# Optimization experiments

Hardware: AMD Instinct MI355X
Metric: run time of the kernel (lower is better)

Reference implementation:

```python
import jax, jax.numpy as jnp
import numpy as np

D_MODEL = 2048
D_STATE = 64
D_CONV = 4
EXPAND = 2
HEADDIM = 64
NGROUPS = 1
CHUNK = 64
D_INNER = D_MODEL * EXPAND          # 4096
NHEADS = D_INNER // HEADDIM         # 64
D_IN_PROJ = 2 * D_INNER + 2 * NGROUPS * D_STATE + NHEADS
BATCH, SEQLEN = 2, 4096
RMS_EPS = 1e-6


def elu_plus_one(x):
    return jax.nn.elu(x) + 1.0


def softplus(x):
    return jnp.where(x > 20, x, jnp.log1p(jnp.exp(x)))


def causal_conv1d(x, w, b):
    # x: (B, L, D), w: (K, D) depthwise kernel, b: (D,)
    Bsz, L, Dn = x.shape
    k = w.shape[0]
    xp = jnp.transpose(jnp.pad(x, ((0, 0), (k - 1, 0), (0, 0))), (0, 2, 1))  # (B, D, L+K-1)
    kern = jnp.transpose(w, (1, 0))[:, None, :]  # (D, 1, K)
    y = jax.lax.conv_general_dilated(xp, kern, (1,), 'VALID',
                                     feature_group_count=Dn,
                                     dimension_numbers=('NCH', 'OIH', 'NCH'))
    return jnp.transpose(y, (0, 2, 1)) + b


def ssd_chunked(q, k, v, a, chunk_size):
    # SSD / chunked linear attention with per-step scalar decay.
    # Recurrence: h_t = a_t * h_{t-1} + k_t v_t^T ; y_t = q_t @ h_t
    # q,k: (B,H,L,N); v: (B,H,L,P); a: (B,H,L) in (0,1)
    Bsz, H, L, N = q.shape
    S = chunk_size
    C = L // S
    qc = q.reshape(Bsz, H, C, S, N)
    kc = k.reshape(Bsz, H, C, S, N)
    vc = v.reshape(Bsz, H, C, S, -1)
    la = jnp.log(a).reshape(Bsz, H, C, S)
    cs = jnp.cumsum(la, axis=-1)                 # inclusive cumsum of log-decay within chunk
    causal = jnp.tril(jnp.ones((S, S), bool))
    # decay from position j to i (j<=i): exp(cs_i - cs_j)
    logdec = jnp.where(causal, cs[..., :, None] - cs[..., None, :], -jnp.inf)
    att = jnp.einsum('bhcsn,bhctn->bhcst', qc, kc) * jnp.exp(logdec)
    y_intra = jnp.einsum('bhcst,bhctp->bhcsp', att, vc)
    total = cs[..., -1]                           # (B,H,C) total log-decay per chunk
    k_scaled = kc * jnp.exp(total[..., None, None] - cs[..., None])
    states = jnp.einsum('bhcsn,bhcsp->bhcnp', k_scaled, vc)  # per-chunk state update
    d_t = jnp.moveaxis(jnp.exp(total), 2, 0)      # (C,B,H)
    s_t = jnp.moveaxis(states, 2, 0)              # (C,B,H,N,P)

    def step(h, inp):
        d, s = inp
        return d[..., None, None] * h + s, h      # emit state at chunk start

    _, h_prev = jax.lax.scan(step, jnp.zeros_like(s_t[0]), (d_t, s_t))
    h_prev = jnp.moveaxis(h_prev, 0, 2)           # (B,H,C,N,P)
    y_inter = jnp.einsum('bhcsn,bhcnp->bhcsp', qc * jnp.exp(cs)[..., None], h_prev)
    return (y_intra + y_inter).reshape(Bsz, H, L, -1)


def setup_inputs() -> dict:
    key = jax.random.key(0)
    k0, k1, k2, k3 = jax.random.split(key, 4)
    u = jax.random.normal(k0, (BATCH, SEQLEN, D_MODEL), jnp.float32)
    in_proj_w = jax.random.normal(k1, (D_MODEL, D_IN_PROJ), jnp.float32) / np.sqrt(D_MODEL)
    conv_weight = jax.random.normal(k2, (D_CONV, D_INNER), jnp.float32) / np.sqrt(D_CONV)
    conv_bias = jnp.zeros((D_INNER,), jnp.float32)
    A_log = jnp.log(jnp.linspace(1.0, 16.0, NHEADS)).astype(jnp.float32)
    dt_init = jnp.exp(jnp.linspace(np.log(0.001), np.log(0.1), NHEADS))
    dt_bias = (dt_init + jnp.log(-jnp.expm1(-dt_init))).astype(jnp.float32)
    D_param = jnp.ones((NHEADS,), jnp.float32)
    norm_scale = jnp.ones((D_INNER,), jnp.float32)
    out_proj_w = jax.random.normal(k3, (D_INNER, D_MODEL), jnp.float32) / np.sqrt(D_INNER)
    return dict(u=u, in_proj_w=in_proj_w, conv_weight=conv_weight, conv_bias=conv_bias,
                A_log=A_log, dt_bias=dt_bias, D_param=D_param, norm_scale=norm_scale,
                out_proj_w=out_proj_w)


def reference(u, in_proj_w, conv_weight, conv_bias, A_log, dt_bias, D_param, norm_scale, out_proj_w):
    Bsz, L, _ = u.shape
    zxBCdt = u @ in_proj_w
    splits = [D_INNER, 2 * D_INNER, 2 * D_INNER + NGROUPS * D_STATE, 2 * D_INNER + 2 * NGROUPS * D_STATE]
    z, x, B_proj, C_proj, dt_logits = jnp.split(zxBCdt, splits, axis=-1)
    x = jax.nn.silu(causal_conv1d(x, conv_weight, conv_bias))
    B_mat = elu_plus_one(B_proj.reshape(Bsz, L, NGROUPS, D_STATE))
    C_mat = elu_plus_one(C_proj.reshape(Bsz, L, NGROUPS, D_STATE))
    hpg = NHEADS // NGROUPS
    B_mat = jnp.repeat(B_mat, hpg, axis=2)   # (B,L,H,N)
    C_mat = jnp.repeat(C_mat, hpg, axis=2)
    dt = softplus(dt_logits + dt_bias)        # (B,L,H)
    a = jnp.exp(-dt * jnp.exp(A_log))         # (B,L,H), per-step decay
    x_heads = x.reshape(Bsz, L, NHEADS, HEADDIM)
    q = jnp.transpose(C_mat, (0, 2, 1, 3))
    k = jnp.transpose(B_mat, (0, 2, 1, 3))
    v = jnp.transpose(x_heads, (0, 2, 1, 3))
    a_t = jnp.transpose(a, (0, 2, 1))
    y = ssd_chunked(q, k, v, a_t, CHUNK)
    y = y + D_param[None, :, None, None] * v  # skip connection
    y = jnp.transpose(y, (0, 2, 1, 3)).reshape(Bsz, L, D_INNER)
    y = y * jax.lax.rsqrt(jnp.mean(y * y, axis=-1, keepdims=True) + RMS_EPS) * norm_scale
    y = y * jax.nn.silu(z)
    return y @ out_proj_w
```

## Files before the change

### kernel.cpp

```cpp
#include <hip/hip_runtime.h>
#include <hip/hip_bf16.h>
#include <cstdint>
#include <cstddef>

#define BATCH   2
#define SEQLEN  4096
#define DMODEL  2048
#define DINNER  4096
#define NHEADS  64
#define HEADDIM 64
#define DSTATE  64
#define CHUNK   64
#define NCHUNK  (SEQLEN/CHUNK)
#define DPROJ   8384
#define DPROJ_PAD 8448
#define MTOK    (BATCH*SEQLEN)
#define RMS_EPS 1e-6f

typedef __hip_bfloat16 bf16;
typedef __attribute__((ext_vector_type(8))) short bf16x8;
typedef __attribute__((ext_vector_type(4))) float f32x4;

__device__ __forceinline__ float siluf(float x) { return x / (1.f + expf(-x)); }
__device__ __forceinline__ float to_f(float x) { return x; }
__device__ __forceinline__ float to_f(bf16 x) { return __bfloat162float(x); }
__device__ __forceinline__ float bf2f(short s) { bf16 h; *(short*)&h = s; return __bfloat162float(h); }
__device__ __forceinline__ void from_f(float& d, float x) { d = x; }
__device__ __forceinline__ void from_f(bf16& d, float x) { d = __float2bfloat16(x); }

__device__ __forceinline__ void gload16(const void* g, void* l) {
  __builtin_amdgcn_global_load_lds(
      (const __attribute__((address_space(1))) void*)g,
      (__attribute__((address_space(3))) void*)l, 16, 0, 0);
}

template <typename TC, bool MASK, int KT>
__global__ __launch_bounds__(512, 2) void gemm_u(
    const bf16* __restrict__ A, int lda,
    const bf16* __restrict__ BT, int ldb,
    TC* __restrict__ C, int ldc, int Nvalid, int gx) {
  __shared__ __align__(16) bf16 As[4 * 8192];
  __shared__ __align__(16) bf16 Bs[4 * 8192];
  const int tid  = threadIdx.x;
  const int lane = tid & 63;
  const int w    = tid >> 6;
  const int wm   = w >> 2;
  const int wn   = w & 3;
  const int lr   = lane & 15, lg = lane >> 4;
  const int fo   = 8 * (lg ^ ((lr >> 1) & 3));

  int nwg = gridDim.x;
  int bid = (int)blockIdx.x;
  int idx = (bid & 7) * (nwg >> 3) + (bid >> 3);
  int spos = idx % (8 * gx);
  const int m0 = ((idx / (8 * gx)) * 8 + (spos & 7)) * 256;
  const int n0 = (spos >> 3) * 256;

  const int srow = tid >> 2;
  const int ce   = 8 * ((tid & 3) ^ ((tid >> 3) & 3));
  const bf16* pA0 = A  + (size_t)(m0 + srow)       * lda + ce;
  const bf16* pA1 = A  + (size_t)(m0 + 128 + srow) * lda + ce;
  const bf16* pB0 = BT + (size_t)(n0 + srow)       * ldb + ce;
  const bf16* pB1 = BT + (size_t)(n0 + 128 + srow) * ldb + ce;
  const int wofs = w * 512;
  const int aRd = (wm * 128 + lr) * 32 + fo;
  const int bRd = (wn * 64 + lr) * 32 + fo;

#define STAGE_A(kt) do {                                       \
    bf16* d_ = As + (((kt) & 3) << 13);  int kk_ = (kt) << 5;  \
    gload16(pA0 + kk_, d_ + wofs);                             \
    gload16(pA1 + kk_, d_ + 4096 + wofs);                      \
  } while (0)
#define STAGE_B(kt) do {                                       \
    bf16* d_ = Bs + (((kt) & 3) << 13);  int kk_ = (kt) << 5;  \
    gload16(pB0 + kk_, d_ + wofs);                             \
    gload16(pB1 + kk_, d_ + 4096 + wofs);                      \
  } while (0)

  f32x4 acc[8][4];
#pragma unroll
  for (int m = 0; m < 8; ++m)
#pragma unroll
    for (int n = 0; n < 4; ++n) acc[m][n] = (f32x4){0.f, 0.f, 0.f, 0.f};

#define KBODY(T, DOSTAGE, VMC) do {                                          \
    const bf16* Ab = As + (((T) & 3) << 13);                                 \
    const bf16* Bb = Bs + (((T) & 3) << 13);                                 \
    if (DOSTAGE) { STAGE_A((T) + 3); STAGE_B((T) + 3); }                     \
    bf16x8 bfv[4], af[4], ag[4];                                             \
    _Pragma("unroll")                                                        \
    for (int n = 0; n < 4; ++n) bfv[n] = *(const bf16x8*)&Bb[bRd + n * 512]; \
    _Pragma("unroll")                                                        \
    for (int m = 0; m < 4; ++m) af[m] = *(const bf16x8*)&Ab[aRd + m * 512];  \
    __builtin_amdgcn_sched_barrier(0);                                       \
    _Pragma("unroll")                                                        \
    for (int m = 0; m < 4; ++m) ag[m] = *(const bf16x8*)&Ab[aRd + (m + 4) * 512]; \
    asm volatile("s_waitcnt lgkmcnt(4)" ::: "memory");                       \
    __builtin_amdgcn_sched_barrier(0);                                       \
    __builtin_amdgcn_s_setprio(1);                                           \
    _Pragma("unroll")                                                        \
    for (int m = 0; m < 4; ++m)                                              \
      _Pragma("unroll")                                                      \
      for (int n = 0; n < 4; ++n)                                            \
        acc[m][n] = __builtin_amdgcn_mfma_f32_16x16x32_bf16(af[m], bfv[n], acc[m][n], 0, 0, 0); \
    asm volatile("s_waitcnt lgkmcnt(0)" ::: "memory");                       \
    __builtin_amdgcn_sched_barrier(0);                                       \
    _Pragma("unroll")                                                        \
    for (int m = 0; m < 4; ++m)                                              \
      _Pragma("unroll")                                                      \
      for (int n = 0; n < 4; ++n)                                            \
        acc[m + 4][n] = __builtin_amdgcn_mfma_f32_16x16x32_bf16(ag[m], bfv[n], acc[m + 4][n], 0, 0, 0); \
    __builtin_amdgcn_s_setprio(0);                                           \
    asm volatile("s_waitcnt vmcnt(" #VMC ")" ::: "memory");                  \
    __builtin_amdgcn_s_barrier();                                            \
    __builtin_amdgcn_sched_barrier(0);                                       \
  } while (0)

  STAGE_A(0); STAGE_B(0); STAGE_A(1); STAGE_B(1); STAGE_A(2); STAGE_B(2);
  asm volatile("s_waitcnt vmcnt(8)" ::: "memory");
  __builtin_amdgcn_s_barrier();
  __builtin_amdgcn_sched_barrier(0);

#pragma unroll 4
  for (int t = 0; t < KT - 3; ++t) KBODY(t, true, 8);
  KBODY(KT - 3, false, 4);
  KBODY(KT - 2, false, 0);
  KBODY(KT - 1, false, 0);
#undef KBODY
#undef STAGE_A
#undef STAGE_B

  if constexpr (__is_same(TC, bf16)) {
    bf16* Ws = (w < 4 ? As : Bs) + (w & 3) * 8192;
#pragma unroll
    for (int m = 0; m < 8; ++m)
#pragma unroll
      for (int n = 0; n < 4; ++n)
#pragma unroll
        for (int reg = 0; reg < 4; ++reg) {
          int row = m * 16 + lg * 4 + reg;
          int slot = (n * 2 + (lr >> 3)) ^ (row & 7);
          Ws[row * 64 + slot * 8 + (lr & 7)] = __float2bfloat16(acc[m][n][reg]);
        }
    asm volatile("s_waitcnt lgkmcnt(0)" ::: "memory");
#pragma unroll
    for (int i = 0; i < 16; ++i) {
      int row = i * 8 + (lane >> 3);
      bf16x8 v = *(const bf16x8*)&Ws[row * 64 + ((lane & 7) ^ (lane >> 3)) * 8];
      int gcol = n0 + wn * 64 + (lane & 7) * 8;
      if (!MASK || gcol < Nvalid)
        *(bf16x8*)&((bf16*)C)[(size_t)(m0 + wm * 128 + row) * ldc + gcol] = v;
    }
  } else {
#pragma unroll
    for (int m = 0; m < 8; ++m)
#pragma unroll
      for (int n = 0; n < 4; ++n) {
        int col = n0 + wn * 64 + n * 16 + lr;
        if (MASK && col >= Nvalid) continue;
        size_t rbase = (size_t)(m0 + wm * 128 + m * 16 + lg * 4);
#pragma unroll
        for (int reg = 0; reg < 4; ++reg)
          from_f(C[(rbase + reg) * ldc + col], acc[m][n][reg]);
      }
  }
}

template <typename TC, bool MASK>
__global__ __launch_bounds__(256) void gemm_mfma(
    const bf16* __restrict__ A, int lda,
    const bf16* __restrict__ BT, int ldb,
    TC* __restrict__ C, int ldc, int Kdim, int Nvalid) {
  __shared__ __align__(16) bf16 As[128 * 32];
  __shared__ __align__(16) bf16 Bs[128 * 32];
  const int tid  = threadIdx.x;
  const int lane = tid & 63;
  const int w    = tid >> 6;
  const int m0 = blockIdx.y * 128;
  const int n0 = blockIdx.x * 128;

  const int rs0 = w * 32 + (lane >> 2);
  const int ce  = 8 * ((lane & 3) ^ ((lane >> 2) & 3));
  const int fo  = 8 * ((lane >> 4) ^ (lane & 3));
  const int lr  = lane & 15, lg = lane >> 4;
  const int wr = w >> 1, wc = w & 1;

  f32x4 acc[4][4];
#pragma unroll
  for (int m = 0; m < 4; ++m)
#pragma unroll
    for (int n = 0; n < 4; ++n) acc[m][n] = (f32x4){0.f, 0.f, 0.f, 0.f};

  const size_t arow0 = (size_t)(m0 + rs0) * lda;
  const size_t arow1 = (size_t)(m0 + rs0 + 16) * lda;
  const size_t brow0 = (size_t)(n0 + rs0) * ldb;
  const size_t brow1 = (size_t)(n0 + rs0 + 16) * ldb;
  bf16* lA0 = &As[(w * 2 + 0) * 512];
  bf16* lA1 = &As[(w * 2 + 1) * 512];
  bf16* lB0 = &Bs[(w * 2 + 0) * 512];
  bf16* lB1 = &Bs[(w * 2 + 1) * 512];

  for (int k0 = 0; k0 < Kdim; k0 += 32) {
    __syncthreads();
    gload16(A + arow0 + k0 + ce, lA0);
    gload16(A + arow1 + k0 + ce, lA1);
    gload16(BT + brow0 + k0 + ce, lB0);
    gload16(BT + brow1 + k0 + ce, lB1);
    __syncthreads();
    bf16x8 af[4], bfr[4];
#pragma unroll
    for (int m = 0; m < 4; ++m)
      af[m] = *(const bf16x8*)&As[(wr * 64 + m * 16 + lr) * 32 + fo];
#pragma unroll
    for (int n = 0; n < 4; ++n)
      bfr[n] = *(const bf16x8*)&Bs[(wc * 64 + n * 16 + lr) * 32 + fo];
#pragma unroll
    for (int m = 0; m < 4; ++m)
#pragma unroll
      for (int n = 0; n < 4; ++n)
        acc[m][n] = __builtin_amdgcn_mfma_f32_16x16x32_bf16(af[m], bfr[n], acc[m][n], 0, 0, 0);
  }

#pragma unroll
  for (int m = 0; m < 4; ++m)
#pragma unroll
    for (int n = 0; n < 4; ++n) {
      int col = n0 + wc * 64 + n * 16 + lr;
      if (MASK && col >= Nvalid) continue;
      size_t rbase = (size_t)(m0 + wr * 64 + m * 16 + lg * 4);
#pragma unroll
      for (int reg = 0; reg < 4; ++reg)
        from_f(C[(rbase + reg) * ldc + col], acc[m][n][reg]);
    }
}

__global__ __launch_bounds__(256) void cast_bf16_kernel(
    const float* __restrict__ x, bf16* __restrict__ y) {
  size_t i = ((size_t)blockIdx.x * 256 + threadIdx.x) * 4;
  float4 v = *(const float4*)(x + i);
  y[i + 0] = __float2bfloat16(v.x);
  y[i + 1] = __float2bfloat16(v.y);
  y[i + 2] = __float2bfloat16(v.z);
  y[i + 3] = __float2bfloat16(v.w);
}

__global__ __launch_bounds__(256) void transpose_cast_kernel(
    const float* __restrict__ W, bf16* __restrict__ WT, int N, int K) {
  __shared__ float t[32][33];
  int n0 = blockIdx.x * 32, k0 = blockIdx.y * 32;
  int tx = threadIdx.x & 31, ty = threadIdx.x >> 5;
#pragma unroll
  for (int i = 0; i < 4; ++i) {
    int n = n0 + tx;
    t[ty + i * 8][tx] = (n < N) ? W[(size_t)(k0 + ty + i * 8) * N + n] : 0.f;
  }
  __syncthreads();
#pragma unroll
  for (int i = 0; i < 4; ++i) {
    int nn = ty + i * 8;
    WT[(size_t)(n0 + nn) * K + k0 + tx] = __float2bfloat16(t[tx][nn]);
  }
}

__global__ __launch_bounds__(256) void conv_silu_kernel(
    const bf16* __restrict__ zx, const float* __restrict__ cw,
    const float* __restrict__ cb, bf16* __restrict__ xc) {
  int idx = blockIdx.x * 256 + threadIdx.x;
  int d8 = (idx & 511) * 8;
  int m = idx >> 9;
  int l = m & (SEQLEN - 1);
  int b = m >> 12;
  float acc[8];
#pragma unroll
  for (int j = 0; j < 8; ++j) acc[j] = cb[d8 + j];
#pragma unroll
  for (int k = 0; k < 4; ++k) {
    int li = l - 3 + k;
    if (li >= 0) {
      bf16x8 xv = *(const bf16x8*)&zx[(size_t)(b * SEQLEN + li) * DPROJ + DINNER + d8];
      const float* cwp = cw + k * DINNER + d8;
#pragma unroll
      for (int j = 0; j < 8; ++j) acc[j] += bf2f(xv[j]) * cwp[j];
    }
  }
  bf16x8 o;
#pragma unroll
  for (int j = 0; j < 8; ++j) { bf16 h = __float2bfloat16(siluf(acc[j])); o[j] = *(short*)&h; }
  *(bf16x8*)&xc[(size_t)m * DINNER + d8] = o;
}

__global__ __launch_bounds__(256) void prep_kernel(
    const bf16* __restrict__ zx, const float* __restrict__ A_log,
    const float* __restrict__ dt_bias, bf16* __restrict__ Bmb,
    bf16* __restrict__ Cmb, float* __restrict__ la) {
  int idx = blockIdx.x * 256 + threadIdx.x;
  int j = idx & 63;
  int m = idx >> 6;
  const bf16* row = zx + (size_t)m * DPROJ;
  float bv = to_f(row[2 * DINNER + j]);
  float cv = to_f(row[2 * DINNER + DSTATE + j]);
  float dtl = to_f(row[2 * DINNER + 2 * DSTATE + j]) + dt_bias[j];
  from_f(Bmb[idx], bv > 0.f ? bv + 1.f : expf(bv));
  from_f(Cmb[idx], cv > 0.f ? cv + 1.f : expf(cv));
  float dt = dtl > 20.f ? dtl : log1pf(expf(dtl));
  la[idx] = -dt * expf(A_log[j]);
}

__global__ __launch_bounds__(64) void cumsum_kernel(
    const float* __restrict__ la, float* __restrict__ cs) {
  int bid = blockIdx.x;
  int c = bid & 63, h = (bid >> 6) & 63, b = bid >> 12;
  int s = threadIdx.x;
  __shared__ float lds[64];
  size_t base = (size_t)(b * SEQLEN + c * CHUNK + s) * 64 + h;
  lds[s] = la[base];
  __syncthreads();
  float acc = 0.f;
  for (int t = 0; t <= s; ++t) acc += lds[t];
  cs[base] = acc;
}

__global__ __launch_bounds__(256) void states_mfma(
    const bf16* __restrict__ Bmb, const bf16* __restrict__ xc,
    const float* __restrict__ cs, bf16* __restrict__ st) {
  int bid = blockIdx.x;
  int c = bid & 63, h = (bid >> 6) & 63, b = bid >> 12;
  int m0 = b * SEQLEN + c * CHUNK;
  int tid = threadIdx.x, lane = tid & 63, w = tid >> 6;
  int lr = lane & 15, lg = lane >> 4;
  __shared__ bf16 vT[64 * 72];
  __shared__ bf16 kT[64 * 72];
  int s4 = tid >> 2, c16 = (tid & 3) * 16;
  float cstot = cs[(size_t)(m0 + 63) * 64 + h];
  float ws = expf(cstot - cs[(size_t)(m0 + s4) * 64 + h]);
  {
    union { bf16x8 v[2]; bf16 hh[16]; } u;
    const bf16x8* pv = (const bf16x8*)&xc[(size_t)(m0 + s4) * DINNER + h * 64 + c16];
    u.v[0] = pv[0]; u.v[1] = pv[1];
#pragma unroll
    for (int i = 0; i < 16; ++i) vT[(c16 + i) * 72 + s4] = u.hh[i];
    const bf16x8* pk = (const bf16x8*)&Bmb[(size_t)(m0 + s4) * 64 + c16];
    u.v[0] = pk[0]; u.v[1] = pk[1];
#pragma unroll
    for (int i = 0; i < 16; ++i) kT[(c16 + i) * 72 + s4] = __float2bfloat16(to_f(u.hh[i]) * ws);
  }
  __syncthreads();
  f32x4 acc[4];
#pragma unroll
  for (int ct = 0; ct < 4; ++ct) acc[ct] = (f32x4){0.f, 0.f, 0.f, 0.f};
#pragma unroll
  for (int ks = 0; ks < 2; ++ks) {
    bf16x8 af = *(const bf16x8*)&vT[(w * 16 + lr) * 72 + ks * 32 + lg * 8];
#pragma unroll
    for (int ct = 0; ct < 4; ++ct) {
      bf16x8 bf_ = *(const bf16x8*)&kT[(ct * 16 + lr) * 72 + ks * 32 + lg * 8];
      acc[ct] = __builtin_amdgcn_mfma_f32_16x16x32_bf16(af, bf_, acc[ct], 0, 0, 0);
    }
  }
  size_t ob = (((size_t)(b * NHEADS + h)) * NCHUNK + c) * 4096;
#pragma unroll
  for (int ct = 0; ct < 4; ++ct) {
    int n = ct * 16 + lr;
#pragma unroll
    for (int r = 0; r < 4; ++r) {
      int p = w * 16 + lg * 4 + r;
      from_f(st[ob + (size_t)p * 64 + n], acc[ct][r]);
    }
  }
}

__global__ __launch_bounds__(256) void scan_kernel(
    const float* __restrict__ cs, bf16* __restrict__ st) {
  int bid = blockIdx.x;
  int bh = bid >> 2, qq = bid & 3;
  int b = bh >> 6, h = bh & 63;
  int tid = threadIdx.x;
  __shared__ float dec[64];
  if (tid < 64)
    dec[tid] = expf(cs[(size_t)(b * SEQLEN + tid * CHUNK + 63) * 64 + h]);
  int e0 = qq * 1024 + tid * 4;
  float hr[4] = {0.f, 0.f, 0.f, 0.f};
  size_t base = (size_t)bh * NCHUNK * 4096;
  typedef __attribute__((ext_vector_type(4))) short bf16x4;
  union U { bf16x4 v; bf16 hh[4]; };
  U buf[4];
  buf[0].v = *(bf16x4*)(st + base + 0 * 4096 + e0);
  buf[1].v = *(bf16x4*)(st + base + 1 * 4096 + e0);
  buf[2].v = *(bf16x4*)(st + base + 2 * 4096 + e0);
  __syncthreads();
#pragma unroll 4
  for (int c = 0; c < NCHUNK; ++c) {
    if (c + 3 < NCHUNK)
      buf[(c + 3) & 3].v = *(bf16x4*)(st + base + (size_t)(c + 3) * 4096 + e0);
    float d = dec[c];
    U out;
#pragma unroll
    for (int i = 0; i < 4; ++i) {
      float sv = to_f(buf[c & 3].hh[i]);
      from_f(out.hh[i], hr[i]);
      hr[i] = d * hr[i] + sv;
    }
    *(bf16x4*)(st + base + (size_t)c * 4096 + e0) = out.v;
  }
}

__global__ __launch_bounds__(256) void chunk_out_mfma(
    const bf16* __restrict__ Bmb, const bf16* __restrict__ Cmb,
    const bf16* __restrict__ xc, const float* __restrict__ cs,
    const bf16* __restrict__ st, const float* __restrict__ Dp,
    bf16* __restrict__ zx) {
  int bid = blockIdx.x;
  int c = bid & 63, h = (bid >> 6) & 63, b = bid >> 12;
  int m0 = b * SEQLEN + c * CHUNK;
  int tid = threadIdx.x, lane = tid & 63, w = tid >> 6;
  int lr = lane & 15, lg = lane >> 4;
  __shared__ bf16 qL[64 * 72];
  __shared__ bf16 kL[64 * 72];
  __shared__ bf16 A2[64 * 136];
  __shared__ bf16 B2[64 * 136];
  __shared__ float csl[64];
  int s4 = tid >> 2, c16 = (tid & 3) * 16;

  if (tid < 64) csl[tid] = cs[(size_t)(m0 + tid) * 64 + h];
  {
    const bf16x8* pq = (const bf16x8*)&Cmb[(size_t)(m0 + s4) * 64 + c16];
    *(bf16x8*)&qL[s4 * 72 + c16] = pq[0];
    *(bf16x8*)&qL[s4 * 72 + c16 + 8] = pq[1];
    const bf16x8* pk = (const bf16x8*)&Bmb[(size_t)(m0 + s4) * 64 + c16];
    *(bf16x8*)&kL[s4 * 72 + c16] = pk[0];
    *(bf16x8*)&kL[s4 * 72 + c16 + 8] = pk[1];
  }
  {
    union { bf16x8 v[2]; bf16 hh[16]; } u;
    const bf16x8* pv = (const bf16x8*)&xc[(size_t)(m0 + s4) * DINNER + h * 64 + c16];
    u.v[0] = pv[0]; u.v[1] = pv[1];
#pragma unroll
    for (int i = 0; i < 16; ++i) B2[(c16 + i) * 136 + s4] = u.hh[i];
  }
  {
    size_t hb = (((size_t)(b * NHEADS + h)) * NCHUNK + c) * 4096;
    const bf16x8* ph = (const bf16x8*)&st[hb + (size_t)s4 * 64 + c16];
    *(bf16x8*)&B2[s4 * 136 + 64 + c16] = ph[0];
    *(bf16x8*)&B2[s4 * 136 + 64 + c16 + 8] = ph[1];
  }
  __syncthreads();

  f32x4 acc1[4];
#pragma unroll
  for (int ct = 0; ct < 4; ++ct) acc1[ct] = (f32x4){0.f, 0.f, 0.f, 0.f};
#pragma unroll
  for (int ks = 0; ks < 2; ++ks) {
    bf16x8 af = *(const bf16x8*)&qL[(w * 16 + lr) * 72 + ks * 32 + lg * 8];
#pragma unroll
    for (int ct = 0; ct < 4; ++ct) {
      bf16x8 bf_ = *(const bf16x8*)&kL[(ct * 16 + lr) * 72 + ks * 32 + lg * 8];
      acc1[ct] = __builtin_amdgcn_mfma_f32_16x16x32_bf16(af, bf_, acc1[ct], 0, 0, 0);
    }
  }
  {
    float es = expf(csl[s4]);
    union { bf16x8 v[2]; bf16 hh[16]; } u;
    const bf16x8* pq = (const bf16x8*)&qL[s4 * 72 + c16];
    u.v[0] = pq[0]; u.v[1] = pq[1];
#pragma unroll
    for (int i = 0; i < 16; ++i) u.hh[i] = __float2bfloat16(to_f(u.hh[i]) * es);
    *(bf16x8*)&A2[s4 * 136 + 64 + c16] = u.v[0];
    *(bf16x8*)&A2[s4 * 136 + 64 + c16 + 8] = u.v[1];
  }
#pragma unroll
  for (int ct = 0; ct < 4; ++ct) {
    int t = ct * 16 + lr;
#pragma unroll
    for (int r = 0; r < 4; ++r) {
      int s = w * 16 + lg * 4 + r;
      float val = (t <= s) ? acc1[ct][r] * expf(csl[s] - csl[t]) : 0.f;
      A2[s * 136 + t] = __float2bfloat16(val);
    }
  }
  __syncthreads();

  float Dh = Dp[h];
  f32x4 acc2[4];
#pragma unroll
  for (int ct = 0; ct < 4; ++ct) {
    int p = ct * 16 + lr;
#pragma unroll
    for (int r = 0; r < 4; ++r)
      acc2[ct][r] = Dh * to_f(B2[p * 136 + (w * 16 + lg * 4 + r)]);
  }
#pragma unroll
  for (int ks = 0; ks < 4; ++ks) {
    bf16x8 af = *(const bf16x8*)&A2[(w * 16 + lr) * 136 + ks * 32 + lg * 8];
#pragma unroll
    for (int ct = 0; ct < 4; ++ct) {
      bf16x8 bf_ = *(const bf16x8*)&B2[(ct * 16 + lr) * 136 + ks * 32 + lg * 8];
      acc2[ct] = __builtin_amdgcn_mfma_f32_16x16x32_bf16(af, bf_, acc2[ct], 0, 0, 0);
    }
  }
  __syncthreads();
#pragma unroll
  for (int ct = 0; ct < 4; ++ct) {
    int p = ct * 16 + lr;
#pragma unroll
    for (int r = 0; r < 4; ++r)
      qL[(w * 16 + lg * 4 + r) * 72 + p] = __float2bfloat16(acc2[ct][r]);
  }
  __syncthreads();
  {
    const bf16x8* py = (const bf16x8*)&qL[s4 * 72 + c16];
    bf16x8* pg = (bf16x8*)&zx[(size_t)(m0 + s4) * DPROJ + DINNER + h * 64 + c16];
    pg[0] = py[0]; pg[1] = py[1];
  }
}

__global__ __launch_bounds__(256) void rmsnorm_gate_kernel(
    bf16* __restrict__ zx, const float* __restrict__ scale) {
  int m = blockIdx.x;
  int tid = threadIdx.x;
  bf16* row = zx + (size_t)m * DPROJ;
  float vals[16];
  float ss = 0.f;
#pragma unroll
  for (int g = 0; g < 2; ++g) {
    int d8 = (tid + g * 256) * 8;
    bf16x8 yv = *(const bf16x8*)&row[DINNER + d8];
#pragma unroll
    for (int j = 0; j < 8; ++j) {
      float y = bf2f(yv[j]);
      vals[g * 8 + j] = y;
      ss += y * y;
    }
  }
#pragma unroll
  for (int off = 32; off > 0; off >>= 1) ss += __shfl_down(ss, off, 64);
  __shared__ float red[4];
  if ((tid & 63) == 0) red[tid >> 6] = ss;
  __syncthreads();
  float tot = red[0] + red[1] + red[2] + red[3];
  float inv = rsqrtf(tot / (float)DINNER + RMS_EPS);
#pragma unroll
  for (int g = 0; g < 2; ++g) {
    int d8 = (tid + g * 256) * 8;
    bf16x8 zv = *(const bf16x8*)&row[d8];
    const float* sc = scale + d8;
    bf16x8 o;
#pragma unroll
    for (int j = 0; j < 8; ++j) {
      bf16 hh = __float2bfloat16(vals[g * 8 + j] * inv * sc[j] * siluf(bf2f(zv[j])));
      o[j] = *(short*)&hh;
    }
    *(bf16x8*)&row[DINNER + d8] = o;
  }
}

extern "C" void kernel_launch(void* const* d_in, const int* in_sizes, int n_in,
                              void* d_out, int out_size, void* d_ws, size_t ws_size,
                              hipStream_t stream) {
  const float* u       = (const float*)d_in[0];
  const float* Win     = (const float*)d_in[1];
  const float* cw      = (const float*)d_in[2];
  const float* cb      = (const float*)d_in[3];
  const float* A_log   = (const float*)d_in[4];
  const float* dt_bias = (const float*)d_in[5];
  const float* Dp      = (const float*)d_in[6];
  const float* nscale  = (const float*)d_in[7];
  const float* Wout    = (const float*)d_in[8];
  float* out = (float*)d_out;

  bf16* zx = (bf16*)d_ws;
  bf16* xc = zx + (size_t)MTOK * DPROJ;
  bf16* ub = xc;
  bf16* wT = xc + (size_t)MTOK * DINNER;
  bf16* Bmb = wT + (size_t)DPROJ_PAD * DMODEL;
  bf16* Cmb = Bmb + (size_t)MTOK * 64;
  float* la = (float*)(Cmb + (size_t)MTOK * 64);
  float* cs = la + (size_t)MTOK * 64;
  bf16* st = (bf16*)d_out;

  cast_bf16_kernel<<<(MTOK * DMODEL) / (256 * 4), 256, 0, stream>>>(u, ub);
  transpose_cast_kernel<<<dim3(DPROJ_PAD / 32, DMODEL / 32), 256, 0, stream>>>(Win, wT, DPROJ, DMODEL);
  gemm_u<bf16, false, DMODEL / 32><<<(2 * DINNER / 256) * (MTOK / 256), 512, 0, stream>>>(
      ub, DMODEL, wT, DMODEL, zx, DPROJ, DPROJ, 2 * DINNER / 256);
  gemm_mfma<bf16, true><<<dim3(2, MTOK / 128), 256, 0, stream>>>(
      ub, DMODEL, wT + (size_t)(2 * DINNER) * DMODEL, DMODEL,
      zx + 2 * DINNER, DPROJ, DMODEL, 2 * DINNER + 192 - (2 * DINNER));
  transpose_cast_kernel<<<dim3(DMODEL / 32, DINNER / 32), 256, 0, stream>>>(Wout, wT, DMODEL, DINNER);
  conv_silu_kernel<<<(MTOK * 512) / 256, 256, 0, stream>>>(zx, cw, cb, xc);
  prep_kernel<<<(MTOK * 64) / 256, 256, 0, stream>>>(zx, A_log, dt_bias, Bmb, Cmb, la);
  cumsum_kernel<<<BATCH * NHEADS * NCHUNK, 64, 0, stream>>>(la, cs);
  states_mfma<<<BATCH * NHEADS * NCHUNK, 256, 0, stream>>>(Bmb, xc, cs, st);
  scan_kernel<<<BATCH * NHEADS * 4, 256, 0, stream>>>(cs, st);
  chunk_out_mfma<<<BATCH * NHEADS * NCHUNK, 256, 0, stream>>>(Bmb, Cmb, xc, cs, st, Dp, zx);
  rmsnorm_gate_kernel<<<MTOK, 256, 0, stream>>>(zx, nscale);
  gemm_u<float, false, DINNER / 32><<<(DMODEL / 256) * (MTOK / 256), 512, 0, stream>>>(
      zx + DINNER, DPROJ, wT, DINNER, out, DMODEL, DMODEL, DMODEL / 256);
}
```

Measured before the change: 662.6 us.

## Add 16-wave GEMM for input projection and fuse prep with chunk cumsum

New measurement: 663.9 us. About the same (+0.2%).

```diff
diff --git a/kernel.cpp b/kernel.cpp
--- a/kernel.cpp
+++ b/kernel.cpp
@@ -32,6 +32,103 @@
   __builtin_amdgcn_global_load_lds(
       (const __attribute__((address_space(1))) void*)g,
       (__attribute__((address_space(3))) void*)l, 16, 0, 0);
+}
+
+template <int KT>
+__global__ __launch_bounds__(1024, 4) void gemm_w16(
+    const bf16* __restrict__ A, int lda,
+    const bf16* __restrict__ BT, int ldb,
+    bf16* __restrict__ C, int ldc, int gx) {
+  __shared__ __align__(16) bf16 As[4 * 8192];
+  __shared__ __align__(16) bf16 Bs[4 * 8192];
+  const int tid  = threadIdx.x;
+  const int lane = tid & 63;
+  const int w    = tid >> 6;
+  const int wm   = w >> 2;
+  const int wn   = w & 3;
+  const int lr   = lane & 15, lg = lane >> 4;
+  const int fo   = 8 * (lg ^ ((lr >> 1) & 3));
+
+  int nwg = gridDim.x;
+  int bid = (int)blockIdx.x;
+  int idx = (bid & 7) * (nwg >> 3) + (bid >> 3);
+  int spos = idx % (8 * gx);
+  const int m0 = ((idx / (8 * gx)) * 8 + (spos & 7)) * 256;
+  const int n0 = (spos >> 3) * 256;
+
+  const int srow = tid >> 2;
+  const int ce   = 8 * ((tid & 3) ^ ((tid >> 3) & 3));
+  const bf16* pA = A  + (size_t)(m0 + srow) * lda + ce;
+  const bf16* pB = BT + (size_t)(n0 + srow) * ldb + ce;
+  const int wofs = w * 512;
+  const int aRd = (wm * 64 + lr) * 32 + fo;
+  const int bRd = (wn * 64 + lr) * 32 + fo;
+
+#define STAGE_A(kt) gload16(pA + ((kt) << 5), As + (((kt) & 3) << 13) + wofs)
+#define STAGE_B(kt) gload16(pB + ((kt) << 5), Bs + (((kt) & 3) << 13) + wofs)
+
+  f32x4 acc[4][4];
+#pragma unroll
+  for (int m = 0; m < 4; ++m)
+#pragma unroll
+    for (int n = 0; n < 4; ++n) acc[m][n] = (f32x4){0.f, 0.f, 0.f, 0.f};
+
+#define KBODY(T, DOSTAGE, VMC) do {                                          \
+    const bf16* Ab = As + (((T) & 3) << 13);                                 \
+    const bf16* Bb = Bs + (((T) & 3) << 13);                                 \
+    if (DOSTAGE) { STAGE_A((T) + 3); STAGE_B((T) + 3); }                     \
+    bf16x8 bfv[4], af[4];                                                    \
+    _Pragma("unroll")                                                        \
+    for (int n = 0; n < 4; ++n) bfv[n] = *(const bf16x8*)&Bb[bRd + n * 512]; \
+    _Pragma("unroll")                                                        \
+    for (int m = 0; m < 4; ++m) af[m] = *(const bf16x8*)&Ab[aRd + m * 512];  \
+    asm volatile("s_waitcnt lgkmcnt(0)" ::: "memory");                       \
+    __builtin_amdgcn_sched_barrier(0);                                       \
+    __builtin_amdgcn_s_setprio(1);                                           \
+    _Pragma("unroll")                                                        \
+    for (int m = 0; m < 4; ++m)                                              \
+      _Pragma("unroll")                                                      \
+      for (int n = 0; n < 4; ++n)                                            \
+        acc[m][n] = __builtin_amdgcn_mfma_f32_16x16x32_bf16(af[m], bfv[n], acc[m][n], 0, 0, 0); \
+    __builtin_amdgcn_s_setprio(0);                                           \
+    asm volatile("s_waitcnt vmcnt(" #VMC ")" ::: "memory");                  \
+    __builtin_amdgcn_s_barrier();                                            \
+    __builtin_amdgcn_sched_barrier(0);                                       \
+  } while (0)
+
+  STAGE_A(0); STAGE_B(0); STAGE_A(1); STAGE_B(1); STAGE_A(2); STAGE_B(2);
+  asm volatile("s_waitcnt vmcnt(4)" ::: "memory");
+  __builtin_amdgcn_s_barrier();
+  __builtin_amdgcn_sched_barrier(0);
+
+#pragma unroll 4
+  for (int t = 0; t < KT - 3; ++t) KBODY(t, true, 4);
+  KBODY(KT - 3, false, 2);
+  KBODY(KT - 2, false, 0);
+  KBODY(KT - 1, false, 0);
+#undef KBODY
+#undef STAGE_A
+#undef STAGE_B
+
+  bf16* Ws = (w < 8 ? As : Bs) + (w & 7) * 4096;
+#pragma unroll
+  for (int m = 0; m < 4; ++m)
+#pragma unroll
+    for (int n = 0; n < 4; ++n)
+#pragma unroll
+      for (int reg = 0; reg < 4; ++reg) {
+        int row = m * 16 + lg * 4 + reg;
+        int slot = (n * 2 + (lr >> 3)) ^ (row & 7);
+        Ws[row * 64 + slot * 8 + (lr & 7)] = __float2bfloat16(acc[m][n][reg]);
+      }
+  asm volatile("s_waitcnt lgkmcnt(0)" ::: "memory");
+#pragma unroll
+  for (int i = 0; i < 8; ++i) {
+    int row = i * 8 + (lane >> 3);
+    bf16x8 v = *(const bf16x8*)&Ws[row * 64 + ((lane & 7) ^ (lane >> 3)) * 8];
+    int gcol = n0 + wn * 64 + (lane & 7) * 8;
+    *(bf16x8*)&C[(size_t)(m0 + wm * 64 + row) * ldc + gcol] = v;
+  }
 }
 
 template <typename TC, bool MASK, int KT>
@@ -289,35 +386,63 @@
   *(bf16x8*)&xc[(size_t)m * DINNER + d8] = o;
 }
 
-__global__ __launch_bounds__(256) void prep_kernel(
+__global__ __launch_bounds__(256) void prep_cumsum_kernel(
     const bf16* __restrict__ zx, const float* __restrict__ A_log,
     const float* __restrict__ dt_bias, bf16* __restrict__ Bmb,
-    bf16* __restrict__ Cmb, float* __restrict__ la) {
-  int idx = blockIdx.x * 256 + threadIdx.x;
-  int j = idx & 63;
-  int m = idx >> 6;
-  const bf16* row = zx + (size_t)m * DPROJ;
-  float bv = to_f(row[2 * DINNER + j]);
-  float cv = to_f(row[2 * DINNER + DSTATE + j]);
-  float dtl = to_f(row[2 * DINNER + 2 * DSTATE + j]) + dt_bias[j];
-  from_f(Bmb[idx], bv > 0.f ? bv + 1.f : expf(bv));
-  from_f(Cmb[idx], cv > 0.f ? cv + 1.f : expf(cv));
-  float dt = dtl > 20.f ? dtl : log1pf(expf(dtl));
-  la[idx] = -dt * expf(A_log[j]);
-}
-
-__global__ __launch_bounds__(64) void cumsum_kernel(
-    const float* __restrict__ la, float* __restrict__ cs) {
+    bf16* __restrict__ Cmb, float* __restrict__ cs) {
   int bid = blockIdx.x;
-  int c = bid & 63, h = (bid >> 6) & 63, b = bid >> 12;
-  int s = threadIdx.x;
-  __shared__ float lds[64];
-  size_t base = (size_t)(b * SEQLEN + c * CHUNK + s) * 64 + h;
-  lds[s] = la[base];
-  __syncthreads();
-  float acc = 0.f;
-  for (int t = 0; t <= s; ++t) acc += lds[t];
-  cs[base] = acc;
+  int c = bid & 63, b = bid >> 6;
+  int m0 = b * SEQLEN + c * CHUNK;
+  int tid = threadIdx.x;
+  int s = tid >> 2, grp = (tid & 3) * 16;
+  __shared__ float laT[64 * 65];
+  __shared__ float segs[4][64];
+  const bf16* row = zx + (size_t)(m0 + s) * DPROJ + 2 * DINNER;
+  {
+    union { bf16x8 v[2]; bf16 hh[16]; } u, o;
+    u.v[0] = *(const bf16x8*)&row[grp];
+    u.v[1] = *(const bf16x8*)&row[grp + 8];
+#pragma unroll
+    for (int i = 0; i < 16; ++i) {
+      float bv = to_f(u.hh[i]);
+      from_f(o.hh[i], bv > 0.f ? bv + 1.f : expf(bv));
+    }
+    *(bf16x8*)&Bmb[(size_t)(m0 + s) * 64 + grp] = o.v[0];
+    *(bf16x8*)&Bmb[(size_t)(m0 + s) * 64 + grp + 8] = o.v[1];
+    u.v[0] = *(const bf16x8*)&row[64 + grp];
+    u.v[1] = *(const bf16x8*)&row[64 + grp + 8];
+#pragma unroll
+    for (int i = 0; i < 16; ++i) {
+      float cv = to_f(u.hh[i]);
+      from_f(o.hh[i], cv > 0.f ? cv + 1.f : expf(cv));
+    }
+    *(bf16x8*)&Cmb[(size_t)(m0 + s) * 64 + grp] = o.v[0];
+    *(bf16x8*)&Cmb[(size_t)(m0 + s) * 64 + grp + 8] = o.v[1];
+    u.v[0] = *(const bf16x8*)&row[128 + grp];
+    u.v[1] = *(const bf16x8*)&row[128 + grp + 8];
+#pragma unroll
+    for (int i = 0; i < 16; ++i) {
+      int j = grp + i;
+      float dtl = to_f(u.hh[i]) + dt_bias[j];
+      float dt = dtl > 20.f ? dtl : log1pf(expf(dtl));
+      laT[j * 65 + s] = -dt * expf(A_log[j]);
+    }
+  }
+  __syncthreads();
+  int j = tid & 63, sg = tid >> 6;
+  float p = 0.f;
+#pragma unroll
+  for (int i = 0; i < 16; ++i) p += laT[j * 65 + sg * 16 + i];
+  segs[sg][j] = p;
+  __syncthreads();
+  float off = (sg > 0 ? segs[0][j] : 0.f) + (sg > 1 ? segs[1][j] : 0.f) +
+              (sg > 2 ? segs[2][j] : 0.f);
+  float acc = off;
+#pragma unroll
+  for (int i = 0; i < 16; ++i) {
+    acc += laT[j * 65 + sg * 16 + i];
+    cs[(size_t)(m0 + sg * 16 + i) * 64 + j] = acc;
+  }
 }
 
 __global__ __launch_bounds__(256) void states_mfma(
@@ -573,21 +698,19 @@
   bf16* wT = xc + (size_t)MTOK * DINNER;
   bf16* Bmb = wT + (size_t)DPROJ_PAD * DMODEL;
   bf16* Cmb = Bmb + (size_t)MTOK * 64;
-  float* la = (float*)(Cmb + (size_t)MTOK * 64);
-  float* cs = la + (size_t)MTOK * 64;
+  float* cs = (float*)(Cmb + (size_t)MTOK * 64);
   bf16* st = (bf16*)d_out;
 
   cast_bf16_kernel<<<(MTOK * DMODEL) / (256 * 4), 256, 0, stream>>>(u, ub);
   transpose_cast_kernel<<<dim3(DPROJ_PAD / 32, DMODEL / 32), 256, 0, stream>>>(Win, wT, DPROJ, DMODEL);
-  gemm_u<bf16, false, DMODEL / 32><<<(2 * DINNER / 256) * (MTOK / 256), 512, 0, stream>>>(
-      ub, DMODEL, wT, DMODEL, zx, DPROJ, DPROJ, 2 * DINNER / 256);
+  gemm_w16<DMODEL / 32><<<(2 * DINNER / 256) * (MTOK / 256), 1024, 0, stream>>>(
+      ub, DMODEL, wT, DMODEL, zx, DPROJ, 2 * DINNER / 256);
   gemm_mfma<bf16, true><<<dim3(2, MTOK / 128), 256, 0, stream>>>(
       ub, DMODEL, wT + (size_t)(2 * DINNER) * DMODEL, DMODEL,
-      zx + 2 * DINNER, DPROJ, DMODEL, 2 * DINNER + 192 - (2 * DINNER));
+      zx + 2 * DINNER, DPROJ, DMODEL, 192);
   transpose_cast_kernel<<<dim3(DMODEL / 32, DINNER / 32), 256, 0, stream>>>(Wout, wT, DMODEL, DINNER);
   conv_silu_kernel<<<(MTOK * 512) / 256, 256, 0, stream>>>(zx, cw, cb, xc);
-  prep_kernel<<<(MTOK * 64) / 256, 256, 0, stream>>>(zx, A_log, dt_bias, Bmb, Cmb, la);
-  cumsum_kernel<<<BATCH * NHEADS * NCHUNK, 64, 0, stream>>>(la, cs);
+  prep_cumsum_kernel<<<BATCH * NCHUNK, 256, 0, stream>>>(zx, A_log, dt_bias, Bmb, Cmb, cs);
   states_mfma<<<BATCH * NHEADS * NCHUNK, 256, 0, stream>>>(Bmb, xc, cs, st);
   scan_kernel<<<BATCH * NHEADS * 4, 256, 0, stream>>>(cs, st);
   chunk_out_mfma<<<BATCH * NHEADS * NCHUNK, 256, 0, stream>>>(Bmb, Cmb, xc, cs, st, Dp, zx);
```
